# Kernel tuning notes

Measured on AMD Instinct MI355X. Metric: run time of the kernel, lower is better.

## Reference

```python
import jax, jax.numpy as jnp
import numpy as np

N, T, F = 20000, 8, 128
E = 320000
H_GCN, H_CONV, H_LSTM = 32, 64, 128


def setup_inputs() -> dict:
    key = jax.random.key(0)
    ks = jax.random.split(key, 16)
    s = lambda k, shape: jax.random.normal(k, shape, dtype=jnp.float32) * 0.05
    inp = {
        'x': jax.random.normal(ks[0], (N, T, F), dtype=jnp.float32),
        'edge_index': jax.random.randint(ks[1], (2, E), 0, N, dtype=jnp.int32),
        'gcn_W': s(ks[2], (F, H_GCN)),
        'gcn_b': s(ks[3], (H_GCN,)),
        'conv_W': s(ks[4], (H_CONV, H_GCN, 2)),
        'conv_b': s(ks[5], (H_CONV,)),
        'W_ih': s(ks[6], (4 * H_LSTM, H_CONV)),
        'W_hh': s(ks[7], (4 * H_LSTM, H_LSTM)),
        'b_ih': s(ks[8], (4 * H_LSTM,)),
        'b_hh': s(ks[9], (4 * H_LSTM,)),
        'fc1_W': s(ks[10], (64, H_LSTM)),
        'fc1_b': s(ks[11], (64,)),
        'fc2_W': s(ks[12], (F, 64)),
        'fc2_b': s(ks[13], (F,)),
    }
    return inp


def _forward(x, edge_index, gcn_W, gcn_b, conv_W, conv_b, W_ih, W_hh, b_ih, b_hh, fc1_W, fc1_b, fc2_W, fc2_b):
    n = x.shape[0]
    # ---- GCNConv (PyG semantics: linear, add self-loops, sym-normalized aggregate) ----
    loops = jnp.arange(n, dtype=edge_index.dtype)
    row = jnp.concatenate([edge_index[0], loops])  # source
    col = jnp.concatenate([edge_index[1], loops])  # target
    deg = jax.ops.segment_sum(jnp.ones_like(col, dtype=x.dtype), col, num_segments=n)
    dinv = jax.lax.rsqrt(deg)  # deg >= 1 thanks to self-loops
    norm = dinv[row] * dinv[col]  # [E+N]
    h = jnp.einsum('ntf,fo->nto', x, gcn_W)  # transform once for all timesteps
    msg = h[row] * norm[:, None, None]  # [E+N, T, 32]
    agg = jax.ops.segment_sum(msg, col, num_segments=n) + gcn_b
    g = jax.nn.relu(agg)  # [N, T, 32]; dropout is identity at inference
    # ---- Conv1d(32->64, k=2) over time ----
    xc = jnp.transpose(g, (0, 2, 1))  # [N, 32, T]
    y = jax.lax.conv_general_dilated(xc, conv_W, window_strides=(1,), padding='VALID',
                                     dimension_numbers=('NCH', 'OIH', 'NCH'))
    y = jax.nn.relu(y + conv_b[None, :, None])  # [N, 64, T-1]
    seq = jnp.transpose(y, (2, 0, 1))  # [T-1, N, 64]
    # ---- LSTM (torch gate order i, f, g, o) ----
    def step(carry, xt):
        hp, cp = carry
        z = xt @ W_ih.T + hp @ W_hh.T + (b_ih + b_hh)  # [N, 4H]
        i, f, gg, o = jnp.split(z, 4, axis=-1)
        c = jax.nn.sigmoid(f) * cp + jax.nn.sigmoid(i) * jnp.tanh(gg)
        hn = jax.nn.sigmoid(o) * jnp.tanh(c)
        return (hn, c), None
    h0 = jnp.zeros((n, H_LSTM), dtype=x.dtype)
    (hT, _), _ = jax.lax.scan(step, (h0, h0), seq)
    # ---- Head ----
    out = jax.nn.relu(hT @ fc1_W.T + fc1_b)
    out = jax.nn.sigmoid(out @ fc2_W.T + fc2_b)
    return out  # [N, num_features]


def reference(x, edge_index, gcn_W, gcn_b, conv_W, conv_b, W_ih, W_hh, b_ih, b_hh, fc1_W, fc1_b, fc2_W, fc2_b):
    return _forward(x, edge_index, gcn_W, gcn_b, conv_W, conv_b, W_ih, W_hh, b_ih, b_hh, fc1_W, fc1_b, fc2_W, fc2_b)
```

## Files before the change

### kernel.cpp

```cpp
#include <hip/hip_runtime.h>
#include <hip/hip_bf16.h>

#define T_STEPS 8
#define F_IN    128
#define H_GCN   32
#define H_CONV  64
#define H_LSTM  128

typedef __bf16 bf16x8 __attribute__((ext_vector_type(8)));
typedef float  f32x4  __attribute__((ext_vector_type(4)));
typedef unsigned short ushort8v __attribute__((ext_vector_type(8)));

#if __has_builtin(__builtin_amdgcn_exp2f)
__device__ __forceinline__ float exp2_f(float x) { return __builtin_amdgcn_exp2f(x); }
#else
__device__ __forceinline__ float exp2_f(float x) { return exp2f(x); }
#endif
#if __has_builtin(__builtin_amdgcn_rcpf)
__device__ __forceinline__ float rcp_f(float x) { return __builtin_amdgcn_rcpf(x); }
#else
__device__ __forceinline__ float rcp_f(float x) { return 1.f / x; }
#endif

#define NL2E  (-1.442695041f)
#define NL2E2 (-2.885390082f)

__device__ __forceinline__ float sigm_fast(float x) {
  return rcp_f(1.f + exp2_f(x * NL2E));
}

__device__ __forceinline__ float ubf(unsigned short u) {
  union { unsigned int i; float f; } v; v.i = ((unsigned int)u) << 16; return v.f;
}
__device__ __forceinline__ unsigned short bfb(float f) {
  __hip_bfloat16 b = __float2bfloat16(f);
  return __builtin_bit_cast(unsigned short, b);
}

__device__ __forceinline__ bf16x8 load_bf8(const __hip_bfloat16* p) {
  int4 v = *reinterpret_cast<const int4*>(p);
  return __builtin_bit_cast(bf16x8, v);
}

__global__ __launch_bounds__(256) void k_transform(const float* __restrict__ x,
                                                   const __hip_bfloat16* __restrict__ Wgt,
                                                   const float* __restrict__ dinv,
                                                   __hip_bfloat16* __restrict__ hs)
{
  int tid  = threadIdx.x;
  int wave = tid >> 6;
  int lane = tid & 63;
  int l15  = lane & 15;
  int lhi  = lane >> 4;
  long r0  = (long)blockIdx.x * 64 + wave * 16;

  bf16x8 bw[2][4];
  #pragma unroll
  for (int ct = 0; ct < 2; ++ct)
    #pragma unroll
    for (int ks = 0; ks < 4; ++ks)
      bw[ct][ks] = load_bf8(Wgt + (ct * 16 + l15) * 128 + ks * 32 + lhi * 8);

  const float* xp = x + (r0 + l15) * 128 + lhi * 8;
  f32x4 acc[2];
  acc[0] = (f32x4){0.f, 0.f, 0.f, 0.f};
  acc[1] = (f32x4){0.f, 0.f, 0.f, 0.f};

  #pragma unroll
  for (int ks = 0; ks < 4; ++ks) {
    float4 v0 = *reinterpret_cast<const float4*>(xp + ks * 32);
    float4 v1 = *reinterpret_cast<const float4*>(xp + ks * 32 + 4);
    bf16x8 a;
    a[0] = (__bf16)v0.x; a[1] = (__bf16)v0.y; a[2] = (__bf16)v0.z; a[3] = (__bf16)v0.w;
    a[4] = (__bf16)v1.x; a[5] = (__bf16)v1.y; a[6] = (__bf16)v1.z; a[7] = (__bf16)v1.w;
    acc[0] = __builtin_amdgcn_mfma_f32_16x16x32_bf16(a, bw[0][ks], acc[0], 0, 0, 0);
    acc[1] = __builtin_amdgcn_mfma_f32_16x16x32_bf16(a, bw[1][ks], acc[1], 0, 0, 0);
  }

  #pragma unroll
  for (int r = 0; r < 4; ++r) {
    long rr = r0 + lhi * 4 + r;
    float dv = dinv[rr >> 3];
    hs[rr * 32 + l15]      = __float2bfloat16(acc[0][r] * dv);
    hs[rr * 32 + 16 + l15] = __float2bfloat16(acc[1][r] * dv);
  }
}

__global__ void k_count_init(const int* __restrict__ col, int* __restrict__ cnt, int E,
                             int* __restrict__ adj, int N, int padE,
                             unsigned int* __restrict__ hz)
{
  int i = blockIdx.x * 256 + threadIdx.x;
  if (i < E) atomicAdd(&cnt[col[i]], 1);
  if (i < padE) adj[i] = N;
  int j = i - padE;
  if (j >= 0 && j < 128) hz[j] = 0u;
}

__global__ __launch_bounds__(1024) void k_scan(const int* __restrict__ cnt,
                                               int* __restrict__ row_ptr,
                                               int* __restrict__ cursor,
                                               float* __restrict__ dinv, int N)
{
  __shared__ int s[1024];
  int tid = threadIdx.x;
  const int CH = (N + 1023) >> 10;
  int i0 = tid * CH;
  int sum = 0;
  for (int j = 0; j < CH; ++j) {
    int i = i0 + j;
    if (i < N) sum += (cnt[i] + 15) & ~15;
  }
  s[tid] = sum;
  __syncthreads();
  #pragma unroll
  for (int off = 1; off < 1024; off <<= 1) {
    int t = (tid >= off) ? s[tid - off] : 0;
    __syncthreads();
    s[tid] += t;
    __syncthreads();
  }
  int run = (tid > 0) ? s[tid - 1] : 0;
  for (int j = 0; j < CH; ++j) {
    int i = i0 + j;
    if (i < N) {
      int v = cnt[i];
      cursor[i] = run;
      row_ptr[i] = run;
      dinv[i] = rsqrtf((float)v + 1.0f);
      run += (v + 15) & ~15;
      if (i == N - 1) row_ptr[N] = run;
    }
  }
}

__global__ void k_fill(const int* __restrict__ ei, int* __restrict__ cursor,
                       int* __restrict__ adj, int E)
{
  int e = blockIdx.x * 256 + threadIdx.x;
  if (e < E) {
    int r = ei[e], c = ei[E + e];
    int pos = atomicAdd(&cursor[c], 1);
    adj[pos] = r;
  }
}

__device__ __forceinline__ void gat16(const int* __restrict__ adj, int base,
                                      const __hip_bfloat16* __restrict__ hl,
                                      float& a0, float& a1, float& a2, float& a3)
{
  int s0 = adj[base + 0],  s1 = adj[base + 1],  s2 = adj[base + 2],  s3 = adj[base + 3];
  int s4 = adj[base + 4],  s5 = adj[base + 5],  s6 = adj[base + 6],  s7 = adj[base + 7];
  int s8 = adj[base + 8],  s9 = adj[base + 9],  sa = adj[base + 10], sb = adj[base + 11];
  int sc = adj[base + 12], sd = adj[base + 13], se = adj[base + 14], sf = adj[base + 15];
  ushort4 r0 = *reinterpret_cast<const ushort4*>(hl + (size_t)s0 * 256);
  ushort4 r1 = *reinterpret_cast<const ushort4*>(hl + (size_t)s1 * 256);
  ushort4 r2 = *reinterpret_cast<const ushort4*>(hl + (size_t)s2 * 256);
  ushort4 r3 = *reinterpret_cast<const ushort4*>(hl + (size_t)s3 * 256);
  ushort4 r4 = *reinterpret_cast<const ushort4*>(hl + (size_t)s4 * 256);
  ushort4 r5 = *reinterpret_cast<const ushort4*>(hl + (size_t)s5 * 256);
  ushort4 r6 = *reinterpret_cast<const ushort4*>(hl + (size_t)s6 * 256);
  ushort4 r7 = *reinterpret_cast<const ushort4*>(hl + (size_t)s7 * 256);
  ushort4 r8 = *reinterpret_cast<const ushort4*>(hl + (size_t)s8 * 256);
  ushort4 r9 = *reinterpret_cast<const ushort4*>(hl + (size_t)s9 * 256);
  ushort4 ra = *reinterpret_cast<const ushort4*>(hl + (size_t)sa * 256);
  ushort4 rb = *reinterpret_cast<const ushort4*>(hl + (size_t)sb * 256);
  ushort4 rc = *reinterpret_cast<const ushort4*>(hl + (size_t)sc * 256);
  ushort4 rd = *reinterpret_cast<const ushort4*>(hl + (size_t)sd * 256);
  ushort4 re = *reinterpret_cast<const ushort4*>(hl + (size_t)se * 256);
  ushort4 rf = *reinterpret_cast<const ushort4*>(hl + (size_t)sf * 256);
  a0 += ((ubf(r0.x) + ubf(r1.x)) + (ubf(r2.x) + ubf(r3.x))) + ((ubf(r4.x) + ubf(r5.x)) + (ubf(r6.x) + ubf(r7.x)))
      + ((ubf(r8.x) + ubf(r9.x)) + (ubf(ra.x) + ubf(rb.x))) + ((ubf(rc.x) + ubf(rd.x)) + (ubf(re.x) + ubf(rf.x)));
  a1 += ((ubf(r0.y) + ubf(r1.y)) + (ubf(r2.y) + ubf(r3.y))) + ((ubf(r4.y) + ubf(r5.y)) + (ubf(r6.y) + ubf(r7.y)))
      + ((ubf(r8.y) + ubf(r9.y)) + (ubf(ra.y) + ubf(rb.y))) + ((ubf(rc.y) + ubf(rd.y)) + (ubf(re.y) + ubf(rf.y)));
  a2 += ((ubf(r0.z) + ubf(r1.z)) + (ubf(r2.z) + ubf(r3.z))) + ((ubf(r4.z) + ubf(r5.z)) + (ubf(r6.z) + ubf(r7.z)))
      + ((ubf(r8.z) + ubf(r9.z)) + (ubf(ra.z) + ubf(rb.z))) + ((ubf(rc.z) + ubf(rd.z)) + (ubf(re.z) + ubf(rf.z)));
  a3 += ((ubf(r0.w) + ubf(r1.w)) + (ubf(r2.w) + ubf(r3.w))) + ((ubf(r4.w) + ubf(r5.w)) + (ubf(r6.w) + ubf(r7.w)))
      + ((ubf(r8.w) + ubf(r9.w)) + (ubf(ra.w) + ubf(rb.w))) + ((ubf(rc.w) + ubf(rd.w)) + (ubf(re.w) + ubf(rf.w)));
}

__global__ __launch_bounds__(256) void k_gather(
    const int* __restrict__ row_ptr, const int* __restrict__ adj,
    const float* __restrict__ dinv, const __hip_bfloat16* __restrict__ hs,
    const float* __restrict__ gcnb,
    __hip_bfloat16* __restrict__ g, int N)
{
  int tid  = threadIdx.x;
  int wave = tid >> 6;
  int lane = tid & 63;

  int na = blockIdx.x * 8 + wave * 2;
  int nb = na + 1;
  int pa = row_ptr[na], ea = row_ptr[na + 1];
  int pb = row_ptr[nb], eb = row_ptr[nb + 1];
  float da = dinv[na], db = dinv[nb];

  const __hip_bfloat16* hl = hs + lane * 4;
  float a0, a1, a2, a3, b0, b1, b2, b3;
  {
    ushort4 hva = *reinterpret_cast<const ushort4*>(hl + (size_t)na * 256);
    ushort4 hvb = *reinterpret_cast<const ushort4*>(hl + (size_t)nb * 256);
    a0 = ubf(hva.x); a1 = ubf(hva.y); a2 = ubf(hva.z); a3 = ubf(hva.w);
    b0 = ubf(hvb.x); b1 = ubf(hvb.y); b2 = ubf(hvb.z); b3 = ubf(hvb.w);
  }

  while (pa < ea && pb < eb) {
    gat16(adj, pa, hl, a0, a1, a2, a3);
    gat16(adj, pb, hl, b0, b1, b2, b3);
    pa += 16; pb += 16;
  }
  while (pa < ea) { gat16(adj, pa, hl, a0, a1, a2, a3); pa += 16; }
  while (pb < eb) { gat16(adj, pb, hl, b0, b1, b2, b3); pb += 16; }

  int ci0 = (lane * 4) & 31;
  float g0 = gcnb[ci0 + 0], g1 = gcnb[ci0 + 1], g2 = gcnb[ci0 + 2], g3 = gcnb[ci0 + 3];
  ushort4 oa, ob;
  oa.x = bfb(fmaxf(fmaf(a0, da, g0), 0.f));
  oa.y = bfb(fmaxf(fmaf(a1, da, g1), 0.f));
  oa.z = bfb(fmaxf(fmaf(a2, da, g2), 0.f));
  oa.w = bfb(fmaxf(fmaf(a3, da, g3), 0.f));
  ob.x = bfb(fmaxf(fmaf(b0, db, g0), 0.f));
  ob.y = bfb(fmaxf(fmaf(b1, db, g1), 0.f));
  ob.z = bfb(fmaxf(fmaf(b2, db, g2), 0.f));
  ob.w = bfb(fmaxf(fmaf(b3, db, g3), 0.f));
  *reinterpret_cast<ushort4*>(g + (size_t)na * 256 + lane * 4) = oa;
  *reinterpret_cast<ushort4*>(g + (size_t)nb * 256 + lane * 4) = ob;
}

__global__ __launch_bounds__(256) void k_conv(
    const __hip_bfloat16* __restrict__ g,
    const __hip_bfloat16* __restrict__ Wcb,
    const float* __restrict__ bc,
    __hip_bfloat16* __restrict__ seq, int N)
{
  __shared__ __hip_bfloat16 A[4][16][72];
  int tid  = threadIdx.x;
  int wave = tid >> 6;
  int lane = tid & 63;
  int l15  = lane & 15;
  int lhi  = lane >> 4;

  if (tid < 144) {
    int w = tid / 36, q = tid % 36;
    int row = 14 + q / 18, cc = (q % 18) * 4;
    *reinterpret_cast<uint2*>(&A[w][row][cc]) = make_uint2(0u, 0u);
  }

  {
    int f0 = tid * 8;
    ushort8v v = *reinterpret_cast<const ushort8v*>(g + (size_t)blockIdx.x * 2048 + f0);
    int n_local = f0 >> 8;
    int rem     = f0 & 255;
    int t_row   = rem >> 5;
    int ci0     = rem & 31;
    int w       = n_local >> 1;
    int rbase   = (n_local & 1) * 7;
    #pragma unroll
    for (int e = 0; e < 8; ++e) {
      unsigned short u = v[e];
      int k0 = (ci0 + e) * 2;
      if (t_row <= 6)
        *reinterpret_cast<unsigned short*>(&A[w][rbase + t_row][k0]) = u;
      if (t_row >= 1)
        *reinterpret_cast<unsigned short*>(&A[w][rbase + t_row - 1][k0 + 1]) = u;
    }
  }
  __syncthreads();

  bf16x8 bfr[2][4];
  #pragma unroll
  for (int ks = 0; ks < 2; ++ks)
    #pragma unroll
    for (int cg = 0; cg < 4; ++cg)
      bfr[ks][cg] = load_bf8(Wcb + (cg * 16 + l15) * 64 + ks * 32 + lhi * 8);

  f32x4 acc[4];
  #pragma unroll
  for (int cg = 0; cg < 4; ++cg) acc[cg] = (f32x4){0.f, 0.f, 0.f, 0.f};

  #pragma unroll
  for (int ks = 0; ks < 2; ++ks) {
    bf16x8 a = load_bf8(&A[wave][l15][ks * 32 + lhi * 8]);
    #pragma unroll
    for (int cg = 0; cg < 4; ++cg)
      acc[cg] = __builtin_amdgcn_mfma_f32_16x16x32_bf16(a, bfr[ks][cg], acc[cg], 0, 0, 0);
  }

  long n64 = (long)N * 64;
  #pragma unroll
  for (int r = 0; r < 4; ++r) {
    int rr = lhi * 4 + r;
    if (rr < 14) {
      int hi = rr >= 7 ? 1 : 0;
      int nl = wave * 2 + hi;
      int t  = rr - 7 * hi;
      long n = (long)blockIdx.x * 8 + nl;
      #pragma unroll
      for (int cg = 0; cg < 4; ++cg) {
        int co = cg * 16 + l15;
        seq[(long)t * n64 + n * 64 + co] = __float2bfloat16(fmaxf(acc[cg][r] + bc[co], 0.f));
      }
    }
  }
}

__global__ __launch_bounds__(256) void k_prep(const float* __restrict__ Wih, const float* __restrict__ Whh,
                       const float* __restrict__ bih, const float* __restrict__ bhh,
                       const float* __restrict__ fc1W, const float* __restrict__ fc2W,
                       const float* __restrict__ convW, const float* __restrict__ gcnW,
                       __hip_bfloat16* __restrict__ Wcat, float* __restrict__ bias,
                       __hip_bfloat16* __restrict__ W1b, __hip_bfloat16* __restrict__ W2b,
                       __hip_bfloat16* __restrict__ Wcb, __hip_bfloat16* __restrict__ Wgt)
{
  int i = blockIdx.x * 256 + threadIdx.x;
  if (i < 512 * 192) {
    int q = i / 192, k = i - q * 192;
    float v = (k < 64) ? Wih[q * 64 + k] : Whh[q * 128 + (k - 64)];
    Wcat[i] = __float2bfloat16(v);
  } else if (i < 512 * 192 + 64 * 128) {
    int j = i - 512 * 192;
    W1b[j] = __float2bfloat16(fc1W[j]);
  } else if (i < 512 * 192 + 64 * 128 + 128 * 64) {
    int j = i - 512 * 192 - 64 * 128;
    W2b[j] = __float2bfloat16(fc2W[j]);
  } else if (i < 512 * 192 + 64 * 128 + 128 * 64 + 64 * 64) {
    int j = i - 512 * 192 - 64 * 128 - 128 * 64;
    Wcb[j] = __float2bfloat16(convW[j]);
  } else if (i < 512 * 192 + 64 * 128 + 128 * 64 + 64 * 64 + 32 * 128) {
    int j = i - 512 * 192 - 64 * 128 - 128 * 64 - 64 * 64;
    int o = j >> 7, f = j & 127;
    Wgt[j] = __float2bfloat16(gcnW[f * 32 + o]);
  } else if (i < 512 * 192 + 64 * 128 + 128 * 64 + 64 * 64 + 32 * 128 + 512) {
    int j = i - 512 * 192 - 64 * 128 - 128 * 64 - 64 * 64 - 32 * 128;
    bias[j] = bih[j] + bhh[j];
  }
}

__global__ __launch_bounds__(512, 2) void k_lstm_head(
    const __hip_bfloat16* __restrict__ seq,
    const __hip_bfloat16* __restrict__ Wcat,
    const float* __restrict__ bias,
    const __hip_bfloat16* __restrict__ W1b,
    const float* __restrict__ fc1b,
    const __hip_bfloat16* __restrict__ W2b,
    const float* __restrict__ fc2b,
    float* __restrict__ out, int N)
{
  __shared__ __hip_bfloat16 h_lds[2][80][136];
  __shared__ __hip_bfloat16 s1_lds[80][72];
  int tid  = threadIdx.x;
  int wave = tid >> 6;
  int lane = tid & 63;
  int l15  = lane & 15;
  int lhi  = lane >> 4;
  long n0  = (long)blockIdx.x * 80;
  int hc   = wave * 16 + l15;

  bf16x8 bw[6][4];
  #pragma unroll
  for (int ks = 0; ks < 6; ++ks)
    #pragma unroll
    for (int gg = 0; gg < 4; ++gg)
      bw[ks][gg] = load_bf8(Wcat + (size_t)(gg * 128 + hc) * 192 + ks * 32 + lhi * 8);

  float kbi = bias[hc]       * NL2E;
  float kbf = bias[128 + hc] * NL2E;
  float kbg = bias[256 + hc] * NL2E2;
  float kbo = bias[384 + hc] * NL2E;
  float c[5][4];
  #pragma unroll
  for (int g = 0; g < 5; ++g)
    #pragma unroll
    for (int r = 0; r < 4; ++r) c[g][r] = 0.f;

  size_t tstr = (size_t)N * 64;
  const __hip_bfloat16* spb = seq + (n0 + l15) * 64 + lhi * 8;

  for (int t = 0; t < 7; ++t) {
    f32x4 acc[5][4];
    #pragma unroll
    for (int g = 0; g < 5; ++g)
      #pragma unroll
      for (int gg = 0; gg < 4; ++gg)
        acc[g][gg] = (f32x4){0.f, 0.f, 0.f, 0.f};

    #pragma unroll
    for (int g = 0; g < 5; ++g) {
      const __hip_bfloat16* sp = spb + (size_t)t * tstr + (size_t)g * 16 * 64;
      bf16x8 a0 = load_bf8(sp);
      bf16x8 a1 = load_bf8(sp + 32);
      #pragma unroll
      for (int gg = 0; gg < 4; ++gg)
        acc[g][gg] = __builtin_amdgcn_mfma_f32_16x16x32_bf16(a0, bw[0][gg], acc[g][gg], 0, 0, 0);
      #pragma unroll
      for (int gg = 0; gg < 4; ++gg)
        acc[g][gg] = __builtin_amdgcn_mfma_f32_16x16x32_bf16(a1, bw[1][gg], acc[g][gg], 0, 0, 0);
    }

    if (t > 0) {
      const __hip_bfloat16* hb = &h_lds[(t + 1) & 1][0][0];
      #pragma unroll
      for (int ks = 2; ks < 6; ++ks) {
        #pragma unroll
        for (int g = 0; g < 5; ++g) {
          bf16x8 a = load_bf8(hb + (g * 16 + l15) * 136 + (ks - 2) * 32 + lhi * 8);
          #pragma unroll
          for (int gg = 0; gg < 4; ++gg)
            acc[g][gg] = __builtin_amdgcn_mfma_f32_16x16x32_bf16(a, bw[ks][gg], acc[g][gg], 0, 0, 0);
        }
      }
    }

    __hip_bfloat16* hw = &h_lds[t & 1][0][0];
    #pragma unroll
    for (int g = 0; g < 5; ++g) {
      #pragma unroll
      for (int r = 0; r < 4; ++r) {
        float si  = rcp_f(1.f + exp2_f(fmaf(acc[g][0][r], NL2E,  kbi)));
        float sf  = rcp_f(1.f + exp2_f(fmaf(acc[g][1][r], NL2E,  kbf)));
        float sg2 = rcp_f(1.f + exp2_f(fmaf(acc[g][2][r], NL2E2, kbg)));
        float so  = rcp_f(1.f + exp2_f(fmaf(acc[g][3][r], NL2E,  kbo)));
        float tg  = fmaf(2.f, sg2, -1.f);
        float cn  = fmaf(sf, c[g][r], si * tg);
        c[g][r] = cn;
        float sc2 = rcp_f(1.f + exp2_f(cn * NL2E2));
        hw[(g * 16 + lhi * 4 + r) * 136 + hc] = __float2bfloat16(so * fmaf(2.f, sc2, -1.f));
      }
    }
    __syncthreads();
  }

  if (wave < 4) {
    int col1 = wave * 16 + l15;
    float b1 = fc1b[col1];
    #pragma unroll
    for (int g = 0; g < 5; ++g) {
      f32x4 acc1v = (f32x4){0.f, 0.f, 0.f, 0.f};
      #pragma unroll
      for (int ks = 0; ks < 4; ++ks) {
        int kb = ks * 32 + lhi * 8;
        bf16x8 a = load_bf8(&h_lds[0][g * 16 + l15][kb]);
        bf16x8 b = load_bf8(W1b + col1 * 128 + kb);
        acc1v = __builtin_amdgcn_mfma_f32_16x16x32_bf16(a, b, acc1v, 0, 0, 0);
      }
      #pragma unroll
      for (int r = 0; r < 4; ++r)
        s1_lds[g * 16 + lhi * 4 + r][col1] = __float2bfloat16(fmaxf(acc1v[r] + b1, 0.f));
    }
  }
  __syncthreads();

  {
    int c2 = wave * 16 + l15;
    float b2 = fc2b[c2];
    #pragma unroll
    for (int g = 0; g < 5; ++g) {
      f32x4 acc2 = (f32x4){0.f, 0.f, 0.f, 0.f};
      #pragma unroll
      for (int ks = 0; ks < 2; ++ks) {
        int kb = ks * 32 + lhi * 8;
        bf16x8 a = load_bf8(&s1_lds[g * 16 + l15][kb]);
        bf16x8 b = load_bf8(W2b + c2 * 64 + kb);
        acc2 = __builtin_amdgcn_mfma_f32_16x16x32_bf16(a, b, acc2, 0, 0, 0);
      }
      #pragma unroll
      for (int r = 0; r < 4; ++r)
        out[(n0 + g * 16 + lhi * 4 + r) * 128 + c2] = sigm_fast(acc2[r] + b2);
    }
  }
}

extern "C" void kernel_launch(void* const* d_in, const int* in_sizes, int n_in,
                              void* d_out, int out_size, void* d_ws, size_t ws_size,
                              hipStream_t stream)
{
  const float* x     = (const float*)d_in[0];
  const int*   ei    = (const int*)d_in[1];
  const float* gcnW  = (const float*)d_in[2];
  const float* gcnb  = (const float*)d_in[3];
  const float* convW = (const float*)d_in[4];
  const float* convb = (const float*)d_in[5];
  const float* Wih   = (const float*)d_in[6];
  const float* Whh   = (const float*)d_in[7];
  const float* bih   = (const float*)d_in[8];
  const float* bhh   = (const float*)d_in[9];
  const float* fc1W  = (const float*)d_in[10];
  const float* fc1b  = (const float*)d_in[11];
  const float* fc2W  = (const float*)d_in[12];
  const float* fc2b  = (const float*)d_in[13];

  const int N = in_sizes[0] / (T_STEPS * F_IN);
  const int E = in_sizes[1] / 2;
  const int padE = E + 16 * N;

  char* ws = (char*)d_ws;
  size_t off = 0;
  auto alloc = [&](size_t bytes) {
    void* p = ws + off;
    off = (off + bytes + 255) & ~(size_t)255;
    return p;
  };
  __hip_bfloat16* hs  = (__hip_bfloat16*)alloc((size_t)(N + 1) * 256 * 2);
  __hip_bfloat16* g   = (__hip_bfloat16*)alloc((size_t)N * 256 * 2);
  __hip_bfloat16* seq = (__hip_bfloat16*)alloc((size_t)7 * N * 64 * 2);
  int* cnt     = (int*)alloc((size_t)N * 4);
  int* row_ptr = (int*)alloc((size_t)(N + 1) * 4);
  int* cursor  = (int*)alloc((size_t)N * 4);
  float* dinv  = (float*)alloc((size_t)N * 4);
  int* adj     = (int*)alloc((size_t)padE * 4);
  __hip_bfloat16* Wcat = (__hip_bfloat16*)alloc(512 * 192 * 2);
  float* bias = (float*)alloc(512 * 4);
  __hip_bfloat16* W1b = (__hip_bfloat16*)alloc(64 * 128 * 2);
  __hip_bfloat16* W2b = (__hip_bfloat16*)alloc(128 * 64 * 2);
  __hip_bfloat16* Wcb = (__hip_bfloat16*)alloc(64 * 64 * 2);
  __hip_bfloat16* Wgt = (__hip_bfloat16*)alloc(32 * 128 * 2);

  hipMemsetAsync(cnt, 0, (size_t)N * 4, stream);

  const int PREP_TOT = 512 * 192 + 64 * 128 + 128 * 64 + 64 * 64 + 32 * 128 + 512;
  k_prep<<<(PREP_TOT + 255) / 256, 256, 0, stream>>>(Wih, Whh, bih, bhh, fc1W, fc2W, convW, gcnW,
                                                     Wcat, bias, W1b, W2b, Wcb, Wgt);
  k_count_init<<<(padE + 128 + 255) / 256, 256, 0, stream>>>(
      ei + E, cnt, E, adj, N, padE, (unsigned int*)(hs + (size_t)N * 256));
  k_scan<<<1, 1024, 0, stream>>>(cnt, row_ptr, cursor, dinv, N);
  k_transform<<<(N * T_STEPS) / 64, 256, 0, stream>>>(x, Wgt, dinv, hs);
  k_fill<<<(E + 255) / 256, 256, 0, stream>>>(ei, cursor, adj, E);
  k_gather<<<N / 8, 256, 0, stream>>>(row_ptr, adj, dinv, hs, gcnb, g, N);
  k_conv<<<N / 8, 256, 0, stream>>>(g, Wcb, convb, seq, N);
  k_lstm_head<<<N / 80, 512, 0, stream>>>(seq, Wcat, bias, W1b, fc1b, W2b, fc2b, (float*)d_out, N);
}
```

Before: 206.8 us.

## Fuse weight prep with degree count, fuse gather with conv, drop CSR padding

Merges the weight-conversion kernel into the degree-count kernel and fuses the GCN gather with the Conv1d kernel, so the aggregated features stay in shared memory instead of taking a global round trip. It also removes the 16-aligned padding of the CSR adjacency. Out-of-range neighbor slots are now masked to a zero row inside the gather, which saves filling the padded adjacency array. This cuts two kernel launches and some memory traffic. In exchange, unaligned segment reads may cross between neighboring rows, and each gather gains extra select instructions.

```diff
diff --git a/kernel.cpp b/kernel.cpp
--- a/kernel.cpp
+++ b/kernel.cpp
@@ -42,6 +42,8 @@
   return __builtin_bit_cast(bf16x8, v);
 }
 
+#define PREP_TOT (512*192 + 64*128 + 128*64 + 64*64 + 32*128 + 512)
+
 __global__ __launch_bounds__(256) void k_transform(const float* __restrict__ x,
                                                    const __hip_bfloat16* __restrict__ Wgt,
                                                    const float* __restrict__ dinv,
@@ -86,15 +88,41 @@
   }
 }
 
-__global__ void k_count_init(const int* __restrict__ col, int* __restrict__ cnt, int E,
-                             int* __restrict__ adj, int N, int padE,
-                             unsigned int* __restrict__ hz)
+__global__ __launch_bounds__(256) void k_prep_count(
+    const int* __restrict__ col, int* __restrict__ cnt, int E,
+    const float* __restrict__ Wih, const float* __restrict__ Whh,
+    const float* __restrict__ bih, const float* __restrict__ bhh,
+    const float* __restrict__ fc1W, const float* __restrict__ fc2W,
+    const float* __restrict__ convW, const float* __restrict__ gcnW,
+    __hip_bfloat16* __restrict__ Wcat, float* __restrict__ bias,
+    __hip_bfloat16* __restrict__ W1b, __hip_bfloat16* __restrict__ W2b,
+    __hip_bfloat16* __restrict__ Wcb, __hip_bfloat16* __restrict__ Wgt,
+    unsigned int* __restrict__ hz)
 {
   int i = blockIdx.x * 256 + threadIdx.x;
   if (i < E) atomicAdd(&cnt[col[i]], 1);
-  if (i < padE) adj[i] = N;
-  int j = i - padE;
-  if (j >= 0 && j < 128) hz[j] = 0u;
+  if (i < 128) hz[i] = 0u;
+  if (i < 512 * 192) {
+    int q = i / 192, k = i - q * 192;
+    float v = (k < 64) ? Wih[q * 64 + k] : Whh[q * 128 + (k - 64)];
+    Wcat[i] = __float2bfloat16(v);
+  } else if (i < 512 * 192 + 64 * 128) {
+    int j = i - 512 * 192;
+    W1b[j] = __float2bfloat16(fc1W[j]);
+  } else if (i < 512 * 192 + 64 * 128 + 128 * 64) {
+    int j = i - 512 * 192 - 64 * 128;
+    W2b[j] = __float2bfloat16(fc2W[j]);
+  } else if (i < 512 * 192 + 64 * 128 + 128 * 64 + 64 * 64) {
+    int j = i - 512 * 192 - 64 * 128 - 128 * 64;
+    Wcb[j] = __float2bfloat16(convW[j]);
+  } else if (i < 512 * 192 + 64 * 128 + 128 * 64 + 64 * 64 + 32 * 128) {
+    int j = i - 512 * 192 - 64 * 128 - 128 * 64 - 64 * 64;
+    int o = j >> 7, f = j & 127;
+    Wgt[j] = __float2bfloat16(gcnW[f * 32 + o]);
+  } else if (i < PREP_TOT) {
+    int j = i - (PREP_TOT - 512);
+    bias[j] = bih[j] + bhh[j];
+  }
 }
 
 __global__ __launch_bounds__(1024) void k_scan(const int* __restrict__ cnt,
@@ -109,7 +137,7 @@
   int sum = 0;
   for (int j = 0; j < CH; ++j) {
     int i = i0 + j;
-    if (i < N) sum += (cnt[i] + 15) & ~15;
+    if (i < N) sum += cnt[i];
   }
   s[tid] = sum;
   __syncthreads();
@@ -128,7 +156,7 @@
       cursor[i] = run;
       row_ptr[i] = run;
       dinv[i] = rsqrtf((float)v + 1.0f);
-      run += (v + 15) & ~15;
+      run += v;
       if (i == N - 1) row_ptr[N] = run;
     }
   }
@@ -145,14 +173,23 @@
   }
 }
 
-__device__ __forceinline__ void gat16(const int* __restrict__ adj, int base,
+__device__ __forceinline__ void gat16(const int* __restrict__ adj, int base, int end, int NN,
                                       const __hip_bfloat16* __restrict__ hl,
                                       float& a0, float& a1, float& a2, float& a3)
 {
+  int lim = end - base;
   int s0 = adj[base + 0],  s1 = adj[base + 1],  s2 = adj[base + 2],  s3 = adj[base + 3];
   int s4 = adj[base + 4],  s5 = adj[base + 5],  s6 = adj[base + 6],  s7 = adj[base + 7];
   int s8 = adj[base + 8],  s9 = adj[base + 9],  sa = adj[base + 10], sb = adj[base + 11];
   int sc = adj[base + 12], sd = adj[base + 13], se = adj[base + 14], sf = adj[base + 15];
+  s0 = (0  < lim) ? s0 : NN;  s1 = (1  < lim) ? s1 : NN;
+  s2 = (2  < lim) ? s2 : NN;  s3 = (3  < lim) ? s3 : NN;
+  s4 = (4  < lim) ? s4 : NN;  s5 = (5  < lim) ? s5 : NN;
+  s6 = (6  < lim) ? s6 : NN;  s7 = (7  < lim) ? s7 : NN;
+  s8 = (8  < lim) ? s8 : NN;  s9 = (9  < lim) ? s9 : NN;
+  sa = (10 < lim) ? sa : NN;  sb = (11 < lim) ? sb : NN;
+  sc = (12 < lim) ? sc : NN;  sd = (13 < lim) ? sd : NN;
+  se = (14 < lim) ? se : NN;  sf = (15 < lim) ? sf : NN;
   ushort4 r0 = *reinterpret_cast<const ushort4*>(hl + (size_t)s0 * 256);
   ushort4 r1 = *reinterpret_cast<const ushort4*>(hl + (size_t)s1 * 256);
   ushort4 r2 = *reinterpret_cast<const ushort4*>(hl + (size_t)s2 * 256);
@@ -179,15 +216,26 @@
       + ((ubf(r8.w) + ubf(r9.w)) + (ubf(ra.w) + ubf(rb.w))) + ((ubf(rc.w) + ubf(rd.w)) + (ubf(re.w) + ubf(rf.w)));
 }
 
-__global__ __launch_bounds__(256) void k_gather(
+__global__ __launch_bounds__(256) void k_gather_conv(
     const int* __restrict__ row_ptr, const int* __restrict__ adj,
     const float* __restrict__ dinv, const __hip_bfloat16* __restrict__ hs,
     const float* __restrict__ gcnb,
-    __hip_bfloat16* __restrict__ g, int N)
-{
+    const __hip_bfloat16* __restrict__ Wcb, const float* __restrict__ bc,
+    __hip_bfloat16* __restrict__ seq, int N)
+{
+  __shared__ __hip_bfloat16 g_lds[8 * 256];
+  __shared__ __hip_bfloat16 A[4][16][72];
   int tid  = threadIdx.x;
   int wave = tid >> 6;
   int lane = tid & 63;
+  int l15  = lane & 15;
+  int lhi  = lane >> 4;
+
+  if (tid < 144) {
+    int w = tid / 36, q = tid % 36;
+    int row = 14 + q / 18, cc = (q % 18) * 4;
+    *reinterpret_cast<uint2*>(&A[w][row][cc]) = make_uint2(0u, 0u);
+  }
 
   int na = blockIdx.x * 8 + wave * 2;
   int nb = na + 1;
@@ -205,12 +253,12 @@
   }
 
   while (pa < ea && pb < eb) {
-    gat16(adj, pa, hl, a0, a1, a2, a3);
-    gat16(adj, pb, hl, b0, b1, b2, b3);
+    gat16(adj, pa, ea, N, hl, a0, a1, a2, a3);
+    gat16(adj, pb, eb, N, hl, b0, b1, b2, b3);
     pa += 16; pb += 16;
   }
-  while (pa < ea) { gat16(adj, pa, hl, a0, a1, a2, a3); pa += 16; }
-  while (pb < eb) { gat16(adj, pb, hl, b0, b1, b2, b3); pb += 16; }
+  while (pa < ea) { gat16(adj, pa, ea, N, hl, a0, a1, a2, a3); pa += 16; }
+  while (pb < eb) { gat16(adj, pb, eb, N, hl, b0, b1, b2, b3); pb += 16; }
 
   int ci0 = (lane * 4) & 31;
   float g0 = gcnb[ci0 + 0], g1 = gcnb[ci0 + 1], g2 = gcnb[ci0 + 2], g3 = gcnb[ci0 + 3];
@@ -223,42 +271,23 @@
   ob.y = bfb(fmaxf(fmaf(b1, db, g1), 0.f));
   ob.z = bfb(fmaxf(fmaf(b2, db, g2), 0.f));
   ob.w = bfb(fmaxf(fmaf(b3, db, g3), 0.f));
-  *reinterpret_cast<ushort4*>(g + (size_t)na * 256 + lane * 4) = oa;
-  *reinterpret_cast<ushort4*>(g + (size_t)nb * 256 + lane * 4) = ob;
-}
-
-__global__ __launch_bounds__(256) void k_conv(
-    const __hip_bfloat16* __restrict__ g,
-    const __hip_bfloat16* __restrict__ Wcb,
-    const float* __restrict__ bc,
-    __hip_bfloat16* __restrict__ seq, int N)
-{
-  __shared__ __hip_bfloat16 A[4][16][72];
-  int tid  = threadIdx.x;
-  int wave = tid >> 6;
-  int lane = tid & 63;
-  int l15  = lane & 15;
-  int lhi  = lane >> 4;
-
-  if (tid < 144) {
-    int w = tid / 36, q = tid % 36;
-    int row = 14 + q / 18, cc = (q % 18) * 4;
-    *reinterpret_cast<uint2*>(&A[w][row][cc]) = make_uint2(0u, 0u);
-  }
+  *reinterpret_cast<ushort4*>(&g_lds[(wave * 2 + 0) * 256 + lane * 4]) = oa;
+  *reinterpret_cast<ushort4*>(&g_lds[(wave * 2 + 1) * 256 + lane * 4]) = ob;
+  __syncthreads();
 
   {
     int f0 = tid * 8;
-    ushort8v v = *reinterpret_cast<const ushort8v*>(g + (size_t)blockIdx.x * 2048 + f0);
+    ushort8v v = *reinterpret_cast<const ushort8v*>(&g_lds[f0]);
     int n_local = f0 >> 8;
     int rem     = f0 & 255;
     int t_row   = rem >> 5;
-    int ci0     = rem & 31;
+    int ci      = rem & 31;
     int w       = n_local >> 1;
     int rbase   = (n_local & 1) * 7;
     #pragma unroll
     for (int e = 0; e < 8; ++e) {
       unsigned short u = v[e];
-      int k0 = (ci0 + e) * 2;
+      int k0 = (ci + e) * 2;
       if (t_row <= 6)
         *reinterpret_cast<unsigned short*>(&A[w][rbase + t_row][k0]) = u;
       if (t_row >= 1)
@@ -301,38 +330,6 @@
         seq[(long)t * n64 + n * 64 + co] = __float2bfloat16(fmaxf(acc[cg][r] + bc[co], 0.f));
       }
     }
-  }
-}
-
-__global__ __launch_bounds__(256) void k_prep(const float* __restrict__ Wih, const float* __restrict__ Whh,
-                       const float* __restrict__ bih, const float* __restrict__ bhh,
-                       const float* __restrict__ fc1W, const float* __restrict__ fc2W,
-                       const float* __restrict__ convW, const float* __restrict__ gcnW,
-                       __hip_bfloat16* __restrict__ Wcat, float* __restrict__ bias,
-                       __hip_bfloat16* __restrict__ W1b, __hip_bfloat16* __restrict__ W2b,
-                       __hip_bfloat16* __restrict__ Wcb, __hip_bfloat16* __restrict__ Wgt)
-{
-  int i = blockIdx.x * 256 + threadIdx.x;
-  if (i < 512 * 192) {
-    int q = i / 192, k = i - q * 192;
-    float v = (k < 64) ? Wih[q * 64 + k] : Whh[q * 128 + (k - 64)];
-    Wcat[i] = __float2bfloat16(v);
-  } else if (i < 512 * 192 + 64 * 128) {
-    int j = i - 512 * 192;
-    W1b[j] = __float2bfloat16(fc1W[j]);
-  } else if (i < 512 * 192 + 64 * 128 + 128 * 64) {
-    int j = i - 512 * 192 - 64 * 128;
-    W2b[j] = __float2bfloat16(fc2W[j]);
-  } else if (i < 512 * 192 + 64 * 128 + 128 * 64 + 64 * 64) {
-    int j = i - 512 * 192 - 64 * 128 - 128 * 64;
-    Wcb[j] = __float2bfloat16(convW[j]);
-  } else if (i < 512 * 192 + 64 * 128 + 128 * 64 + 64 * 64 + 32 * 128) {
-    int j = i - 512 * 192 - 64 * 128 - 128 * 64 - 64 * 64;
-    int o = j >> 7, f = j & 127;
-    Wgt[j] = __float2bfloat16(gcnW[f * 32 + o]);
-  } else if (i < 512 * 192 + 64 * 128 + 128 * 64 + 64 * 64 + 32 * 128 + 512) {
-    int j = i - 512 * 192 - 64 * 128 - 128 * 64 - 64 * 64 - 32 * 128;
-    bias[j] = bih[j] + bhh[j];
   }
 }
 
@@ -491,7 +488,6 @@
 
   const int N = in_sizes[0] / (T_STEPS * F_IN);
   const int E = in_sizes[1] / 2;
-  const int padE = E + 16 * N;
 
   char* ws = (char*)d_ws;
   size_t off = 0;
@@ -501,13 +497,12 @@
     return p;
   };
   __hip_bfloat16* hs  = (__hip_bfloat16*)alloc((size_t)(N + 1) * 256 * 2);
-  __hip_bfloat16* g   = (__hip_bfloat16*)alloc((size_t)N * 256 * 2);
   __hip_bfloat16* seq = (__hip_bfloat16*)alloc((size_t)7 * N * 64 * 2);
   int* cnt     = (int*)alloc((size_t)N * 4);
   int* row_ptr = (int*)alloc((size_t)(N + 1) * 4);
   int* cursor  = (int*)alloc((size_t)N * 4);
   float* dinv  = (float*)alloc((size_t)N * 4);
-  int* adj     = (int*)alloc((size_t)padE * 4);
+  int* adj     = (int*)alloc((size_t)(E + 16) * 4);
   __hip_bfloat16* Wcat = (__hip_bfloat16*)alloc(512 * 192 * 2);
   float* bias = (float*)alloc(512 * 4);
   __hip_bfloat16* W1b = (__hip_bfloat16*)alloc(64 * 128 * 2);
@@ -517,15 +512,13 @@
 
   hipMemsetAsync(cnt, 0, (size_t)N * 4, stream);
 
-  const int PREP_TOT = 512 * 192 + 64 * 128 + 128 * 64 + 64 * 64 + 32 * 128 + 512;
-  k_prep<<<(PREP_TOT + 255) / 256, 256, 0, stream>>>(Wih, Whh, bih, bhh, fc1W, fc2W, convW, gcnW,
-                                                     Wcat, bias, W1b, W2b, Wcb, Wgt);
-  k_count_init<<<(padE + 128 + 255) / 256, 256, 0, stream>>>(
-      ei + E, cnt, E, adj, N, padE, (unsigned int*)(hs + (size_t)N * 256));
+  int pc_work = E > PREP_TOT ? E : PREP_TOT;
+  k_prep_count<<<(pc_work + 255) / 256, 256, 0, stream>>>(
+      ei + E, cnt, E, Wih, Whh, bih, bhh, fc1W, fc2W, convW, gcnW,
+      Wcat, bias, W1b, W2b, Wcb, Wgt, (unsigned int*)(hs + (size_t)N * 256));
   k_scan<<<1, 1024, 0, stream>>>(cnt, row_ptr, cursor, dinv, N);
   k_transform<<<(N * T_STEPS) / 64, 256, 0, stream>>>(x, Wgt, dinv, hs);
   k_fill<<<(E + 255) / 256, 256, 0, stream>>>(ei, cursor, adj, E);
-  k_gather<<<N / 8, 256, 0, stream>>>(row_ptr, adj, dinv, hs, gcnb, g, N);
-  k_conv<<<N / 8, 256, 0, stream>>>(g, Wcb, convb, seq, N);
+  k_gather_conv<<<N / 8, 256, 0, stream>>>(row_ptr, adj, dinv, hs, gcnb, Wcb, convb, seq, N);
   k_lstm_head<<<N / 80, 512, 0, stream>>>(seq, Wcat, bias, W1b, fc1b, W2b, fc2b, (float*)d_out, N);
 }
```

Result: faster. 201.5 us (-2.6%).
